# Performance work log

Hardware: AMD Instinct MI355X
Metric: run time of the kernel (lower is better)

The kernel has to match this reference:

```python
import jax, jax.numpy as jnp
import numpy as np


def _segsum(x):
    """Stable segment sum: exp(segsum(A)) is 1-semiseparable. x: (..., T) -> (..., T, T)."""
    T = x.shape[-1]
    xx = jnp.broadcast_to(x[..., None], (*x.shape, T))
    xx = jnp.where(jnp.tril(jnp.ones((T, T), bool), -1), xx, 0.0)
    s = jnp.cumsum(xx, axis=-2)
    return jnp.where(jnp.tril(jnp.ones((T, T), bool), 0), s, -jnp.inf)


def setup_inputs() -> dict:
    key = jax.random.key(0)
    ks = jax.random.split(key, 6)
    b, T, h, p, n = 2, 1024, 32, 64, 128
    x = jax.random.normal(ks[0], (b, T, h, p), jnp.float32)
    # negative decay rates, as produced by -exp(A_log)*softplus(dt) in Mamba2
    A = -jax.random.uniform(ks[1], (b, T, h), jnp.float32, minval=0.01, maxval=0.5)
    B = jax.random.normal(ks[2], (b, T, h, n), jnp.float32)
    C = jax.random.normal(ks[3], (b, T, h, n), jnp.float32)
    # retrieval similarity mask (lower-triangular, like segment_and_cosine_similarity output)
    L_mask = jax.random.uniform(ks[4], (b, h, T, T), jnp.float32) * jnp.tril(jnp.ones((T, T), jnp.float32))
    mask_scaling_factor = jnp.float32(0.5)
    return {"x": x, "A": A, "B": B, "C": C, "L_mask": L_mask,
            "mask_scaling_factor": mask_scaling_factor, "chunk_size": 64}


def reference(x, A, B, C, L_mask, mask_scaling_factor, chunk_size):
    b, T, h, p = x.shape
    n = B.shape[-1]
    l = chunk_size
    k = T // l
    # chunk: b (c l) ... -> b c l ...
    xr = x.reshape(b, k, l, h, p)
    Br = B.reshape(b, k, l, h, n)
    Cr = C.reshape(b, k, l, h, n)
    Ar = jnp.transpose(A.reshape(b, k, l, h), (0, 3, 1, 2))  # b h c l
    A_cs = jnp.cumsum(Ar, axis=-1)                            # b h c l
    L = jnp.exp(_segsum(Ar))                                  # b h c l l
    # decompose_diagonal_and_lower_tri(L_mask, chunk_size)
    r = L_mask.reshape(b, h, k, l, k, l)
    didx = np.arange(k)
    L_mask_diag = jnp.moveaxis(r[:, :, didx, :, didx, :], 0, 2)          # b h k l l
    row_idx, col_idx = np.tril_indices(k, -1)                             # strict lower block pairs
    lower_tri = jnp.moveaxis(r[:, :, row_idx, :, col_idx, :], 0, 2)       # b h P l l
    L = L + mask_scaling_factor * L_mask_diag
    # diagonal (intra-chunk) blocks
    Y_diag = jnp.einsum('bclhn,bcshn,bhcls,bcshp->bclhp', Cr, Br, L, xr)
    # retrieval off-diagonal blocks, scatter-added back per destination chunk
    Y_tmp = jnp.einsum('bclhn,bcshn,bhcls,bcshp->bclhp',
                       Cr[:, row_idx], Br[:, col_idx],
                       mask_scaling_factor * lower_tri, xr[:, col_idx])   # b P l h p
    Y_retr = jnp.moveaxis(
        jax.ops.segment_sum(jnp.moveaxis(Y_tmp, 1, 0), jnp.asarray(row_idx), num_segments=k),
        0, 1)                                                             # b k l h p
    # inter-chunk state passing
    decay_states = jnp.exp(A_cs[..., -1:] - A_cs)                         # b h c l
    states = jnp.einsum('bclhn,bhcl,bclhp->bchpn', Br, decay_states, xr)  # b c h p n
    states = jnp.concatenate([jnp.zeros_like(states[:, :1]), states], axis=1)
    decay_chunk = jnp.exp(_segsum(jnp.pad(A_cs[..., -1], ((0, 0), (0, 0), (1, 0)))))  # b h (k+1) (k+1)
    new_states = jnp.einsum('bhzc,bchpn->bzhpn', decay_chunk, states)
    states_in, final_state = new_states[:, :-1], new_states[:, -1]
    Y_off = jnp.einsum('bclhn,bchpn,bhcl->bclhp', Cr, states_in, jnp.exp(A_cs))
    Y = (Y_diag + Y_off + Y_retr).reshape(b, T, h, p)
    return Y, final_state
```

## Files before the change

kernel.cpp:

```cpp
#include <hip/hip_runtime.h>

#define T_ 1024
#define H_ 32
#define P_ 64
#define N_ 128
#define L_ 64

typedef float f32x4 __attribute__((ext_vector_type(4)));
typedef short short8 __attribute__((ext_vector_type(8)));
typedef short short4v __attribute__((ext_vector_type(4)));

static __device__ __forceinline__ unsigned short f2bf(float f) {
  unsigned int u = __float_as_uint(f);
  u += 0x7fffu + ((u >> 16) & 1u);
  return (unsigned short)(u >> 16);
}
static __device__ __forceinline__ float bf2f(short s) {
  return __uint_as_float(((unsigned int)(unsigned short)s) << 16);
}

__global__ __launch_bounds__(1024) void cuma_kernel(const float* __restrict__ A,
                                                    float* __restrict__ cumA) {
  const int bh = blockIdx.x;
  const int b = bh >> 5, h = bh & 31;
  const int t = threadIdx.x;
  __shared__ float s[1024];
  s[t] = A[(b * T_ + t) * H_ + h];
  __syncthreads();
  for (int off = 1; off < 1024; off <<= 1) {
    float v = (t >= off) ? s[t - off] : 0.0f;
    __syncthreads();
    s[t] += v;
    __syncthreads();
  }
  cumA[bh * T_ + t] = s[t];
}

__global__ __launch_bounds__(256) void prep_kernel(
    const float* __restrict__ x, const float* __restrict__ Bm,
    const float* __restrict__ Cm, short* __restrict__ Bbf,
    short* __restrict__ BT, short* __restrict__ Cbf,
    short* __restrict__ xT) {
  const int bh = blockIdx.x;
  const int tb = blockIdx.y;
  const int b = bh >> 5, h = bh & 31;
  const int tid = threadIdx.x;
  __shared__ short Bt[128][72];
  __shared__ short Xt[64][72];

#pragma unroll
  for (int i = 0; i < 8; ++i) {
    const int idx = tid + 256 * i;
    const int row = idx >> 5, n4 = idx & 31;
    const float4 v = *(const float4*)(Bm + ((size_t)(b * T_ + tb * 64 + row) * H_ + h) * N_ + n4 * 4);
    short4v o;
    o.x = (short)f2bf(v.x); o.y = (short)f2bf(v.y);
    o.z = (short)f2bf(v.z); o.w = (short)f2bf(v.w);
    *(short4v*)(Bbf + ((size_t)bh * T_ + tb * 64 + row) * N_ + n4 * 4) = o;
    Bt[n4 * 4 + 0][row] = o.x; Bt[n4 * 4 + 1][row] = o.y;
    Bt[n4 * 4 + 2][row] = o.z; Bt[n4 * 4 + 3][row] = o.w;
  }
#pragma unroll
  for (int i = 0; i < 8; ++i) {
    const int idx = tid + 256 * i;
    const int row = idx >> 5, n4 = idx & 31;
    const float4 v = *(const float4*)(Cm + ((size_t)(b * T_ + tb * 64 + row) * H_ + h) * N_ + n4 * 4);
    short4v o;
    o.x = (short)f2bf(v.x); o.y = (short)f2bf(v.y);
    o.z = (short)f2bf(v.z); o.w = (short)f2bf(v.w);
    *(short4v*)(Cbf + ((size_t)bh * T_ + tb * 64 + row) * N_ + n4 * 4) = o;
  }
#pragma unroll
  for (int i = 0; i < 4; ++i) {
    const int idx = tid + 256 * i;
    const int row = idx >> 4, p4 = idx & 15;
    const float4 v = *(const float4*)(x + ((size_t)(b * T_ + tb * 64 + row) * H_ + h) * P_ + p4 * 4);
    Xt[p4 * 4 + 0][row] = (short)f2bf(v.x);
    Xt[p4 * 4 + 1][row] = (short)f2bf(v.y);
    Xt[p4 * 4 + 2][row] = (short)f2bf(v.z);
    Xt[p4 * 4 + 3][row] = (short)f2bf(v.w);
  }
  __syncthreads();
#pragma unroll
  for (int i = 0; i < 4; ++i) {
    const int idx = tid + 256 * i;
    const int n = idx >> 3, t8 = idx & 7;
    const short4v a = *(const short4v*)&Bt[n][t8 * 8];
    const short4v c = *(const short4v*)&Bt[n][t8 * 8 + 4];
    short8 o;
    o[0] = a.x; o[1] = a.y; o[2] = a.z; o[3] = a.w;
    o[4] = c.x; o[5] = c.y; o[6] = c.z; o[7] = c.w;
    *(short8*)(BT + ((size_t)bh * N_ + n) * T_ + tb * 64 + t8 * 8) = o;
  }
#pragma unroll
  for (int i = 0; i < 2; ++i) {
    const int idx = tid + 256 * i;
    const int p = idx >> 3, t8 = idx & 7;
    const short4v a = *(const short4v*)&Xt[p][t8 * 8];
    const short4v c = *(const short4v*)&Xt[p][t8 * 8 + 4];
    short8 o;
    o[0] = a.x; o[1] = a.y; o[2] = a.z; o[3] = a.w;
    o[4] = c.x; o[5] = c.y; o[6] = c.z; o[7] = c.w;
    *(short8*)(xT + ((size_t)bh * P_ + p) * T_ + tb * 64 + t8 * 8) = o;
  }
}

__global__ __launch_bounds__(256, 4) void attn_kernel(
    const short* __restrict__ xT, const short* __restrict__ Bbf,
    const short* __restrict__ Cbf, const float* __restrict__ mask,
    const float* __restrict__ msf_p, const float* __restrict__ cumA,
    float* __restrict__ Y) {
  const int blk = blockIdx.x;
  const int qc = 15 - (blk >> 6);
  const int bh = blk & 63;
  const int b = bh >> 5, h = bh & 31;
  const float msf = msf_p[0];
  const int tid = threadIdx.x;
  const int w = tid >> 6;
  const int lane = tid & 63;
  const int q = lane >> 4, c = lane & 15;

  __shared__ short Ps[4][16][72];

  short8 cf[4];
  {
    const short* Cg = Cbf + ((size_t)bh * T_ + qc * L_ + 16 * w + c) * N_ + 8 * q;
#pragma unroll
    for (int kt = 0; kt < 4; ++kt) cf[kt] = *(const short8*)(Cg + kt * 32);
  }
  float ca_i[4];
#pragma unroll
  for (int r = 0; r < 4; ++r)
    ca_i[r] = cumA[bh * T_ + qc * L_ + 16 * w + 4 * q + r];

  f32x4 yacc[4];
#pragma unroll
  for (int pt = 0; pt < 4; ++pt) yacc[pt] = (f32x4){0.f, 0.f, 0.f, 0.f};

  const float* mrow0 = mask + ((size_t)bh * T_ + (size_t)(qc * L_ + 16 * w + 4 * q)) * T_ + c;

  float mv[16], ck[4];
  {
    const float* mb = mrow0;
#pragma unroll
    for (int tj = 0; tj < 4; ++tj)
#pragma unroll
      for (int r = 0; r < 4; ++r)
        mv[tj * 4 + r] = __builtin_nontemporal_load(mb + (size_t)r * T_ + 16 * tj);
#pragma unroll
    for (int tj = 0; tj < 4; ++tj) ck[tj] = cumA[bh * T_ + 16 * tj + c];
  }

  for (int kc = 0; kc <= qc; ++kc) {
    float mvn[16], ckn[4];
    if (kc < qc) {
      const float* mb = mrow0 + (size_t)(kc + 1) * L_;
#pragma unroll
      for (int tj = 0; tj < 4; ++tj)
#pragma unroll
        for (int r = 0; r < 4; ++r)
          mvn[tj * 4 + r] = __builtin_nontemporal_load(mb + (size_t)r * T_ + 16 * tj);
#pragma unroll
      for (int tj = 0; tj < 4; ++tj)
        ckn[tj] = cumA[bh * T_ + (kc + 1) * L_ + 16 * tj + c];
    }

    f32x4 sacc[4];
#pragma unroll
    for (int tj = 0; tj < 4; ++tj) sacc[tj] = (f32x4){0.f, 0.f, 0.f, 0.f};
    const short* Bg = Bbf + ((size_t)bh * T_ + kc * L_) * N_ + 8 * q;
#pragma unroll
    for (int kt = 0; kt < 4; ++kt) {
#pragma unroll
      for (int tj = 0; tj < 4; ++tj) {
        const short8 bf = *(const short8*)(Bg + (size_t)(16 * tj + c) * N_ + kt * 32);
        sacc[tj] = __builtin_amdgcn_mfma_f32_16x16x32_bf16(cf[kt], bf, sacc[tj], 0, 0, 0);
      }
    }

    const bool diag = (kc == qc);
#pragma unroll
    for (int tj = 0; tj < 4; ++tj) {
      const int j_l = 16 * tj + c;
#pragma unroll
      for (int r = 0; r < 4; ++r) {
        const int i_l = 16 * w + 4 * q + r;
        float wgt = __expf(ca_i[r] - ck[tj]) + msf * mv[tj * 4 + r];
        if (diag && j_l > i_l) wgt = 0.0f;
        Ps[w][4 * q + r][j_l] = (short)f2bf(sacc[tj][r] * wgt);
      }
    }

#pragma unroll
    for (int kt2 = 0; kt2 < 2; ++kt2) {
      const short8 pf = *(const short8*)&Ps[w][c][kt2 * 32 + 8 * q];
      const short* xg = xT + (size_t)bh * P_ * T_ + kc * L_ + kt2 * 32 + 8 * q;
#pragma unroll
      for (int pt = 0; pt < 4; ++pt) {
        const short8 xf = *(const short8*)(xg + (size_t)(16 * pt + c) * T_);
        yacc[pt] = __builtin_amdgcn_mfma_f32_16x16x32_bf16(pf, xf, yacc[pt], 0, 0, 0);
      }
    }

#pragma unroll
    for (int e = 0; e < 16; ++e) mv[e] = mvn[e];
#pragma unroll
    for (int e = 0; e < 4; ++e) ck[e] = ckn[e];
  }

  float* Yg = Y + ((size_t)(b * T_ + qc * L_ + 16 * w + 4 * q) * H_ + h) * P_;
#pragma unroll
  for (int pt = 0; pt < 4; ++pt)
#pragma unroll
    for (int r = 0; r < 4; ++r)
      __builtin_nontemporal_store(yacc[pt][r], Yg + (size_t)r * (H_ * P_) + 16 * pt + c);
}

__global__ __launch_bounds__(512) void state_kernel(
    const short* __restrict__ xT, const short* __restrict__ BT,
    const float* __restrict__ cumA, float* __restrict__ out) {
  const int bh = blockIdx.x;
  const int tid = threadIdx.x;
  const int w = (tid >> 6) & 3;
  const int th = tid >> 8;
  const int lane = tid & 63;
  const int q = lane >> 4, c = lane & 15;

  __shared__ float wsh[1024];
  __shared__ float red[4][16][128];
  {
    const float cend = cumA[bh * T_ + (T_ - 1)];
    for (int t = tid; t < 1024; t += 512)
      wsh[t] = __expf(cend - cumA[bh * T_ + t]);
  }
  __syncthreads();

  f32x4 acc[8];
#pragma unroll
  for (int nt = 0; nt < 8; ++nt) acc[nt] = (f32x4){0.f, 0.f, 0.f, 0.f};

  for (int ktl = 0; ktl < 16; ++ktl) {
    const int t0 = th * 512 + ktl * 32;
    const short8 xv = *(const short8*)(xT + ((size_t)bh * P_ + 16 * w + c) * T_ + t0 + 8 * q);
    const float4 w0 = *(const float4*)&wsh[t0 + 8 * q];
    const float4 w1 = *(const float4*)&wsh[t0 + 8 * q + 4];
    short8 af;
    af[0] = (short)f2bf(bf2f(xv[0]) * w0.x); af[1] = (short)f2bf(bf2f(xv[1]) * w0.y);
    af[2] = (short)f2bf(bf2f(xv[2]) * w0.z); af[3] = (short)f2bf(bf2f(xv[3]) * w0.w);
    af[4] = (short)f2bf(bf2f(xv[4]) * w1.x); af[5] = (short)f2bf(bf2f(xv[5]) * w1.y);
    af[6] = (short)f2bf(bf2f(xv[6]) * w1.z); af[7] = (short)f2bf(bf2f(xv[7]) * w1.w);
#pragma unroll
    for (int nt = 0; nt < 8; ++nt) {
      const short8 bf = *(const short8*)(BT + ((size_t)bh * N_ + 16 * nt + c) * T_ + t0 + 8 * q);
      acc[nt] = __builtin_amdgcn_mfma_f32_16x16x32_bf16(af, bf, acc[nt], 0, 0, 0);
    }
  }

  if (th == 1) {
#pragma unroll
    for (int nt = 0; nt < 8; ++nt)
#pragma unroll
      for (int r = 0; r < 4; ++r) red[w][4 * q + r][16 * nt + c] = acc[nt][r];
  }
  __syncthreads();
  if (th == 0) {
    float* o = out + (size_t)bh * P_ * N_;
#pragma unroll
    for (int nt = 0; nt < 8; ++nt)
#pragma unroll
      for (int r = 0; r < 4; ++r)
        o[(size_t)(16 * w + 4 * q + r) * N_ + 16 * nt + c] =
            acc[nt][r] + red[w][4 * q + r][16 * nt + c];
  }
}

extern "C" void kernel_launch(void* const* d_in, const int* in_sizes, int n_in,
                              void* d_out, int out_size, void* d_ws, size_t ws_size,
                              hipStream_t stream) {
  const float* x    = (const float*)d_in[0];
  const float* A    = (const float*)d_in[1];
  const float* Bm   = (const float*)d_in[2];
  const float* Cm   = (const float*)d_in[3];
  const float* mask = (const float*)d_in[4];
  const float* msf  = (const float*)d_in[5];
  float* Y  = (float*)d_out;
  float* fs = (float*)d_out + (size_t)2 * T_ * H_ * P_;

  char* ws = (char*)d_ws;
  float* cumA = (float*)ws;
  size_t off = 1 << 18;
  short* Bbf = (short*)(ws + off); off += (size_t)64 * T_ * N_ * 2;
  short* BT  = (short*)(ws + off); off += (size_t)64 * T_ * N_ * 2;
  short* Cbf = (short*)(ws + off); off += (size_t)64 * T_ * N_ * 2;
  short* xT  = (short*)(ws + off);

  cuma_kernel<<<64, 1024, 0, stream>>>(A, cumA);
  prep_kernel<<<dim3(64, 16), 256, 0, stream>>>(x, Bm, Cm, Bbf, BT, Cbf, xT);
  attn_kernel<<<1024, 256, 0, stream>>>(xT, Bbf, Cbf, mask, msf, cumA, Y);
  state_kernel<<<64, 512, 0, stream>>>(xT, BT, cumA, fs);
}
```

Baseline: 554.0 us.

## Batch-load B/x fragments per chunk, relax launch bounds, split state kernel with atomics

The attention loop now loads all B and x MFMA fragments for a chunk into registers up front. It manually double-buffers the mask and cumA prefetch by alternating between two register sets, which gives more memory-level parallelism per step. Launch bounds drop from 4 to 2 waves per SIMD so the larger register footprint fits. The final-state kernel is split across 4 time quarters per head with atomicAdd accumulation into a zeroed output, adding a zeroing launch and making the float summation order nondeterministic.

Result: faster. 505.1 us (-8.8%).

```diff
diff --git a/kernel.cpp b/kernel.cpp
--- a/kernel.cpp
+++ b/kernel.cpp
@@ -105,7 +105,7 @@
   }
 }
 
-__global__ __launch_bounds__(256, 4) void attn_kernel(
+__global__ __launch_bounds__(256, 2) void attn_kernel(
     const short* __restrict__ xT, const short* __restrict__ Bbf,
     const short* __restrict__ Cbf, const float* __restrict__ mask,
     const float* __restrict__ msf_p, const float* __restrict__ cumA,
@@ -138,75 +138,75 @@
   for (int pt = 0; pt < 4; ++pt) yacc[pt] = (f32x4){0.f, 0.f, 0.f, 0.f};
 
   const float* mrow0 = mask + ((size_t)bh * T_ + (size_t)(qc * L_ + 16 * w + 4 * q)) * T_ + c;
-
-  float mv[16], ck[4];
-  {
-    const float* mb = mrow0;
-#pragma unroll
-    for (int tj = 0; tj < 4; ++tj)
-#pragma unroll
-      for (int r = 0; r < 4; ++r)
-        mv[tj * 4 + r] = __builtin_nontemporal_load(mb + (size_t)r * T_ + 16 * tj);
-#pragma unroll
-    for (int tj = 0; tj < 4; ++tj) ck[tj] = cumA[bh * T_ + 16 * tj + c];
-  }
-
-  for (int kc = 0; kc <= qc; ++kc) {
-    float mvn[16], ckn[4];
-    if (kc < qc) {
-      const float* mb = mrow0 + (size_t)(kc + 1) * L_;
-#pragma unroll
-      for (int tj = 0; tj < 4; ++tj)
-#pragma unroll
-        for (int r = 0; r < 4; ++r)
-          mvn[tj * 4 + r] = __builtin_nontemporal_load(mb + (size_t)r * T_ + 16 * tj);
-#pragma unroll
-      for (int tj = 0; tj < 4; ++tj)
-        ckn[tj] = cumA[bh * T_ + (kc + 1) * L_ + 16 * tj + c];
-    }
-
-    f32x4 sacc[4];
-#pragma unroll
-    for (int tj = 0; tj < 4; ++tj) sacc[tj] = (f32x4){0.f, 0.f, 0.f, 0.f};
-    const short* Bg = Bbf + ((size_t)bh * T_ + kc * L_) * N_ + 8 * q;
-#pragma unroll
-    for (int kt = 0; kt < 4; ++kt) {
-#pragma unroll
-      for (int tj = 0; tj < 4; ++tj) {
-        const short8 bf = *(const short8*)(Bg + (size_t)(16 * tj + c) * N_ + kt * 32);
-        sacc[tj] = __builtin_amdgcn_mfma_f32_16x16x32_bf16(cf[kt], bf, sacc[tj], 0, 0, 0);
-      }
-    }
-
-    const bool diag = (kc == qc);
-#pragma unroll
-    for (int tj = 0; tj < 4; ++tj) {
-      const int j_l = 16 * tj + c;
-#pragma unroll
-      for (int r = 0; r < 4; ++r) {
-        const int i_l = 16 * w + 4 * q + r;
-        float wgt = __expf(ca_i[r] - ck[tj]) + msf * mv[tj * 4 + r];
-        if (diag && j_l > i_l) wgt = 0.0f;
-        Ps[w][4 * q + r][j_l] = (short)f2bf(sacc[tj][r] * wgt);
-      }
-    }
-
-#pragma unroll
-    for (int kt2 = 0; kt2 < 2; ++kt2) {
-      const short8 pf = *(const short8*)&Ps[w][c][kt2 * 32 + 8 * q];
-      const short* xg = xT + (size_t)bh * P_ * T_ + kc * L_ + kt2 * 32 + 8 * q;
-#pragma unroll
-      for (int pt = 0; pt < 4; ++pt) {
-        const short8 xf = *(const short8*)(xg + (size_t)(16 * pt + c) * T_);
-        yacc[pt] = __builtin_amdgcn_mfma_f32_16x16x32_bf16(pf, xf, yacc[pt], 0, 0, 0);
-      }
-    }
-
-#pragma unroll
-    for (int e = 0; e < 16; ++e) mv[e] = mvn[e];
-#pragma unroll
-    for (int e = 0; e < 4; ++e) ck[e] = ckn[e];
-  }
+  const short* Bg0 = Bbf + (size_t)bh * T_ * N_ + 8 * q;
+  const short* xg0 = xT + (size_t)bh * P_ * T_ + 8 * q;
+
+  float mvA[16], mvB[16], ckA[4], ckB[4];
+#pragma unroll
+  for (int tj = 0; tj < 4; ++tj)
+#pragma unroll
+    for (int r = 0; r < 4; ++r)
+      mvA[tj * 4 + r] = __builtin_nontemporal_load(mrow0 + (size_t)r * T_ + 16 * tj);
+#pragma unroll
+  for (int tj = 0; tj < 4; ++tj) ckA[tj] = cumA[bh * T_ + 16 * tj + c];
+
+#define ATTN_STEP(KC, MVI, CKI, MVO, CKO)                                      \
+  {                                                                            \
+    const int kc_ = (KC);                                                      \
+    const int kcn_ = (kc_ + 1 <= qc) ? (kc_ + 1) : qc;                         \
+    short8 bfr[16];                                                            \
+    const short* Bg = Bg0 + (size_t)kc_ * L_ * N_;                             \
+    _Pragma("unroll") for (int kt = 0; kt < 4; ++kt)                           \
+        _Pragma("unroll") for (int tj = 0; tj < 4; ++tj)                       \
+            bfr[kt * 4 + tj] =                                                 \
+        *(const short8*)(Bg + (size_t)(16 * tj + c) * N_ + kt * 32);           \
+    short8 xfr[8];                                                             \
+    const short* xg = xg0 + kc_ * L_;                                          \
+    _Pragma("unroll") for (int kt2 = 0; kt2 < 2; ++kt2)                        \
+        _Pragma("unroll") for (int pt = 0; pt < 4; ++pt)                       \
+            xfr[kt2 * 4 + pt] =                                                \
+        *(const short8*)(xg + (size_t)(16 * pt + c) * T_ + kt2 * 32);          \
+    const float* mb = mrow0 + (size_t)kcn_ * L_;                               \
+    _Pragma("unroll") for (int tj = 0; tj < 4; ++tj)                           \
+        _Pragma("unroll") for (int r = 0; r < 4; ++r)                          \
+            MVO[tj * 4 + r] =                                                  \
+        __builtin_nontemporal_load(mb + (size_t)r * T_ + 16 * tj);             \
+    _Pragma("unroll") for (int tj = 0; tj < 4; ++tj)                           \
+        CKO[tj] = cumA[bh * T_ + kcn_ * L_ + 16 * tj + c];                     \
+    f32x4 sacc[4];                                                             \
+    _Pragma("unroll") for (int tj = 0; tj < 4; ++tj)                           \
+        sacc[tj] = (f32x4){0.f, 0.f, 0.f, 0.f};                                \
+    _Pragma("unroll") for (int kt = 0; kt < 4; ++kt)                           \
+        _Pragma("unroll") for (int tj = 0; tj < 4; ++tj)                       \
+            sacc[tj] = __builtin_amdgcn_mfma_f32_16x16x32_bf16(                \
+        cf[kt], bfr[kt * 4 + tj], sacc[tj], 0, 0, 0);                          \
+    const bool diag = (kc_ == qc);                                             \
+    _Pragma("unroll") for (int tj = 0; tj < 4; ++tj) {                         \
+      const int j_l = 16 * tj + c;                                             \
+      _Pragma("unroll") for (int r = 0; r < 4; ++r) {                          \
+        const int i_l = 16 * w + 4 * q + r;                                    \
+        float wgt = __expf(ca_i[r] - CKI[tj]) + msf * MVI[tj * 4 + r];         \
+        if (diag && j_l > i_l) wgt = 0.0f;                                     \
+        Ps[w][4 * q + r][j_l] = (short)f2bf(sacc[tj][r] * wgt);                \
+      }                                                                        \
+    }                                                                          \
+    _Pragma("unroll") for (int kt2 = 0; kt2 < 2; ++kt2) {                      \
+      const short8 pf = *(const short8*)&Ps[w][c][kt2 * 32 + 8 * q];           \
+      _Pragma("unroll") for (int pt = 0; pt < 4; ++pt)                         \
+          yacc[pt] = __builtin_amdgcn_mfma_f32_16x16x32_bf16(                  \
+          pf, xfr[kt2 * 4 + pt], yacc[pt], 0, 0, 0);                           \
+    }                                                                          \
+  }
+
+  int kc = 0;
+  for (; kc + 1 <= qc; kc += 2) {
+    ATTN_STEP(kc, mvA, ckA, mvB, ckB)
+    ATTN_STEP(kc + 1, mvB, ckB, mvA, ckA)
+  }
+  if (kc <= qc) {
+    ATTN_STEP(kc, mvA, ckA, mvB, ckB)
+  }
+#undef ATTN_STEP
 
   float* Yg = Y + ((size_t)(b * T_ + qc * L_ + 16 * w + 4 * q) * H_ + h) * P_;
 #pragma unroll
@@ -216,22 +216,25 @@
       __builtin_nontemporal_store(yacc[pt][r], Yg + (size_t)r * (H_ * P_) + 16 * pt + c);
 }
 
-__global__ __launch_bounds__(512) void state_kernel(
+__global__ __launch_bounds__(256) void zero_fs(float* __restrict__ fs) {
+  const int i = blockIdx.x * 256 + threadIdx.x;
+  ((float4*)fs)[i] = make_float4(0.f, 0.f, 0.f, 0.f);
+}
+
+__global__ __launch_bounds__(256) void state_kernel(
     const short* __restrict__ xT, const short* __restrict__ BT,
     const float* __restrict__ cumA, float* __restrict__ out) {
   const int bh = blockIdx.x;
+  const int tq = blockIdx.y;
   const int tid = threadIdx.x;
-  const int w = (tid >> 6) & 3;
-  const int th = tid >> 8;
+  const int w = tid >> 6;
   const int lane = tid & 63;
   const int q = lane >> 4, c = lane & 15;
 
-  __shared__ float wsh[1024];
-  __shared__ float red[4][16][128];
+  __shared__ float wsh[256];
   {
     const float cend = cumA[bh * T_ + (T_ - 1)];
-    for (int t = tid; t < 1024; t += 512)
-      wsh[t] = __expf(cend - cumA[bh * T_ + t]);
+    wsh[tid] = __expf(cend - cumA[bh * T_ + tq * 256 + tid]);
   }
   __syncthreads();
 
@@ -239,9 +242,11 @@
 #pragma unroll
   for (int nt = 0; nt < 8; ++nt) acc[nt] = (f32x4){0.f, 0.f, 0.f, 0.f};
 
-  for (int ktl = 0; ktl < 16; ++ktl) {
-    const int t0 = th * 512 + ktl * 32;
-    const short8 xv = *(const short8*)(xT + ((size_t)bh * P_ + 16 * w + c) * T_ + t0 + 8 * q);
+#pragma unroll
+  for (int ktl = 0; ktl < 8; ++ktl) {
+    const int t0 = ktl * 32;
+    const int tg = tq * 256 + t0;
+    const short8 xv = *(const short8*)(xT + ((size_t)bh * P_ + 16 * w + c) * T_ + tg + 8 * q);
     const float4 w0 = *(const float4*)&wsh[t0 + 8 * q];
     const float4 w1 = *(const float4*)&wsh[t0 + 8 * q + 4];
     short8 af;
@@ -251,27 +256,17 @@
     af[6] = (short)f2bf(bf2f(xv[6]) * w1.z); af[7] = (short)f2bf(bf2f(xv[7]) * w1.w);
 #pragma unroll
     for (int nt = 0; nt < 8; ++nt) {
-      const short8 bf = *(const short8*)(BT + ((size_t)bh * N_ + 16 * nt + c) * T_ + t0 + 8 * q);
+      const short8 bf = *(const short8*)(BT + ((size_t)bh * N_ + 16 * nt + c) * T_ + tg + 8 * q);
       acc[nt] = __builtin_amdgcn_mfma_f32_16x16x32_bf16(af, bf, acc[nt], 0, 0, 0);
     }
   }
 
-  if (th == 1) {
-#pragma unroll
-    for (int nt = 0; nt < 8; ++nt)
-#pragma unroll
-      for (int r = 0; r < 4; ++r) red[w][4 * q + r][16 * nt + c] = acc[nt][r];
-  }
-  __syncthreads();
-  if (th == 0) {
-    float* o = out + (size_t)bh * P_ * N_;
-#pragma unroll
-    for (int nt = 0; nt < 8; ++nt)
-#pragma unroll
-      for (int r = 0; r < 4; ++r)
-        o[(size_t)(16 * w + 4 * q + r) * N_ + 16 * nt + c] =
-            acc[nt][r] + red[w][4 * q + r][16 * nt + c];
-  }
+  float* o = out + (size_t)bh * P_ * N_;
+#pragma unroll
+  for (int nt = 0; nt < 8; ++nt)
+#pragma unroll
+    for (int r = 0; r < 4; ++r)
+      atomicAdd(&o[(size_t)(16 * w + 4 * q + r) * N_ + 16 * nt + c], acc[nt][r]);
 }
 
 extern "C" void kernel_launch(void* const* d_in, const int* in_sizes, int n_in,
@@ -297,5 +292,6 @@
   cuma_kernel<<<64, 1024, 0, stream>>>(A, cumA);
   prep_kernel<<<dim3(64, 16), 256, 0, stream>>>(x, Bm, Cm, Bbf, BT, Cbf, xT);
   attn_kernel<<<1024, 256, 0, stream>>>(xT, Bbf, Cbf, mask, msf, cumA, Y);
-  state_kernel<<<64, 512, 0, stream>>>(xT, BT, cumA, fs);
-}
+  zero_fs<<<512, 256, 0, stream>>>(fs);
+  state_kernel<<<dim3(64, 4), 256, 0, stream>>>(xT, BT, cumA, fs);
+}
```
